# Kernel tuning notes

Measured on AMD Instinct MI355X. Metric: run time of the kernel, lower is better.

## Reference

```python
import jax, jax.numpy as jnp
import numpy as np

DIM = 256
NUM_HEADS = 8
KERNEL_SIZES = [7, 7]
DILATIONS = [1, 2]
NUM_SPLITS = 2
HEAD_DIM = DIM // NUM_HEADS
SCALE = HEAD_DIM ** -0.5


def _window_start(L, K, D):
    """NATTEN get_window_start, vectorized over indices 0..L-1 (static numpy)."""
    idx = np.arange(L)
    NH = K // 2
    if D <= 1:
        return np.maximum(idx - NH, 0) + (idx + NH >= L) * (L - idx - NH - 1)
    ni = idx - NH * D
    imodd = idx % D
    a = (L // D) * D
    b = L - a
    edge = np.where(imodd < b, L - b + imodd - 2 * NH * D, a + imodd - K * D)
    return np.where(ni < 0, imodd, np.where(idx + NH * D >= L, edge, ni))


def _pb_start(L, K, D):
    """NATTEN get_pb_start (relative position bias offset), static numpy."""
    idx = np.arange(L)
    NH = K // 2
    if D <= 1:
        return NH + (idx < NH) * (NH - idx) + (idx + NH >= L) * (L - idx - 1 - NH)
    return np.where(idx - NH * D < 0, K - 1 - idx // D,
                    np.where(idx + NH * D >= L, (L - idx - 1) // D, NH))


def _natten2d(q, k, v, rpb, K, D):
    # q,k,v: [B,h,H,W,d]; rpb: [h, 2K-1, 2K-1]
    B, h, H, W, d = q.shape
    ki = _window_start(H, K, D)[:, None] + D * np.arange(K)   # [H,K]
    kj = _window_start(W, K, D)[:, None] + D * np.arange(K)   # [W,K]
    bi = _pb_start(H, K, D)[:, None] + np.arange(K)           # [H,K]
    bj = _pb_start(W, K, D)[:, None] + np.arange(K)           # [W,K]
    kg = jnp.take(jnp.take(k, ki, axis=2), kj, axis=4)        # [B,h,H,K,W,K,d]
    vg = jnp.take(jnp.take(v, ki, axis=2), kj, axis=4)        # [B,h,H,K,W,K,d]
    attn = jnp.einsum('bhijd,bhiujvd->bhijuv', q, kg)         # [B,h,H,W,K,K]
    bias = jnp.take(jnp.take(rpb, bi, axis=1), bj, axis=3)    # [h,H,K,W,K]
    attn = attn + bias.transpose(0, 1, 3, 2, 4)[None]
    attn = jax.nn.softmax(attn.reshape(B, h, H, W, K * K), axis=-1)
    attn = attn.reshape(B, h, H, W, K, K)
    return jnp.einsum('bhijuv,bhiujvd->bhijd', attn, vg)      # [B,h,H,W,d]


def setup_inputs() -> dict:
    key = jax.random.key(0)
    ks = jax.random.split(key, 6)
    B, C, H, W = 2, DIM, 56, 56
    x = jax.random.normal(ks[0], (B, C, H, W), dtype=jnp.float32)
    w_qkv1 = jax.random.normal(ks[1], (3 * C, C), dtype=jnp.float32) * (C ** -0.5)
    w_qkv2 = jax.random.normal(ks[2], (3 * C, 1, 3, 3), dtype=jnp.float32) * (1.0 / 3.0)
    rpb0 = jax.random.truncated_normal(ks[3], -2.0, 2.0,
                                       (NUM_HEADS // NUM_SPLITS, 13, 13), dtype=jnp.float32) * 0.02
    rpb1 = jax.random.truncated_normal(ks[4], -2.0, 2.0,
                                       (NUM_HEADS // NUM_SPLITS, 13, 13), dtype=jnp.float32) * 0.02
    w_proj = jax.random.normal(ks[5], (C, C), dtype=jnp.float32) * (C ** -0.5)
    return {"x": x, "w_qkv1": w_qkv1, "w_qkv2": w_qkv2,
            "rpb0": rpb0, "rpb1": rpb1, "w_proj": w_proj}


def reference(x, w_qkv1, w_qkv2, rpb0, rpb1, w_proj):
    B, C, H, W = x.shape
    # qkv: 1x1 conv (no bias) then depthwise 3x3 conv (no bias)
    y = jnp.einsum('oc,bchw->bohw', w_qkv1, x)
    y = jax.lax.conv_general_dilated(
        y, w_qkv2, window_strides=(1, 1), padding='SAME',
        dimension_numbers=('NCHW', 'OIHW', 'NCHW'), feature_group_count=3 * C)
    # Faithful to torch: raw reshape of [B,3C,H,W] -> [B,H,W,3,nh,hd]
    qkv = y.reshape(B, H, W, 3, NUM_HEADS, HEAD_DIM).transpose(3, 0, 4, 1, 2, 5)
    q, k, v = qkv[0] * SCALE, qkv[1], qkv[2]   # [B,nh,H,W,hd]
    hs = NUM_HEADS // NUM_SPLITS
    rpbs = [rpb0, rpb1]
    outs = []
    for s in range(NUM_SPLITS):
        sl = slice(s * hs, (s + 1) * hs)
        outs.append(_natten2d(q[:, sl], k[:, sl], v[:, sl],
                              rpbs[s], KERNEL_SIZES[s], DILATIONS[s]))
    o = jnp.concatenate(outs, axis=1)                 # [B,nh,H,W,hd]
    o = o.transpose(0, 1, 4, 2, 3).reshape(B, C, H, W)
    return jnp.einsum('oc,bchw->bohw', w_proj, o)
```

## Files before the change

### kernel.cpp

```cpp
#include <hip/hip_runtime.h>
#include <hip/hip_bf16.h>

#define HGT 56
#define WID 56
#define SPA 3136
#define CCH 256
#define C3  768
#define NH  8
#define HD  32
#define YB  2408448
#define ISTR 43008
#define JSTR 768
#define SCALE_Q 0.17677669529663687f

typedef __attribute__((ext_vector_type(8))) short short8;
typedef __attribute__((ext_vector_type(4))) float f32x4;

static __device__ __forceinline__ unsigned short f2bf_bits(float f) {
    __hip_bfloat16 h = __float2bfloat16(f);
    union { __hip_bfloat16 h; unsigned short u; } cv; cv.h = h; return cv.u;
}
static __device__ __forceinline__ float bf_lo(unsigned u) {
    union { unsigned x; float f; } c; c.x = u << 16; return c.f;
}
static __device__ __forceinline__ float bf_hi(unsigned u) {
    union { unsigned x; float f; } c; c.x = u & 0xffff0000u; return c.f;
}
static __device__ __forceinline__ float bfu(unsigned short u) {
    union { unsigned x; float f; } c; c.x = (unsigned)u << 16; return c.f;
}

__global__ __launch_bounds__(256) void k_cvt(const float* __restrict__ x,
                                             const float* __restrict__ w1,
                                             const float* __restrict__ wp,
                                             __hip_bfloat16* __restrict__ xT,
                                             __hip_bfloat16* __restrict__ w1b,
                                             __hip_bfloat16* __restrict__ wpb) {
    __shared__ __align__(16) __hip_bfloat16 Sl[64][80];
    const int t = threadIdx.x;
    const int z = blockIdx.z;
    if (z == 2) {
        const int gid = (blockIdx.y * 49 + blockIdx.x) * 256 + t;
        for (int i = gid * 4; i < 262144; i += 200704) {
            const float* src;
            __hip_bfloat16* dst;
            if (i < 196608) { src = w1 + i; dst = w1b + i; }
            else            { src = wp + (i - 196608); dst = wpb + (i - 196608); }
            float4 v = *(const float4*)src;
            ushort4 u;
            u.x = f2bf_bits(v.x); u.y = f2bf_bits(v.y);
            u.z = f2bf_bits(v.z); u.w = f2bf_bits(v.w);
            *(ushort4*)dst = u;
        }
        return;
    }
    const int b = z, c0 = blockIdx.y * 64, s0 = blockIdx.x * 64;
    const float* xb = x + (size_t)b * (CCH * SPA);
    const int sq = (t & 15) * 4, cq = (t >> 4) * 4;
    float4 r[4];
#pragma unroll
    for (int rr = 0; rr < 4; ++rr)
        r[rr] = *(const float4*)&xb[(size_t)(c0 + cq + rr) * SPA + s0 + sq];
#pragma unroll
    for (int j = 0; j < 4; ++j) {
        ushort4 u;
        u.x = f2bf_bits(((const float*)&r[0])[j]);
        u.y = f2bf_bits(((const float*)&r[1])[j]);
        u.z = f2bf_bits(((const float*)&r[2])[j]);
        u.w = f2bf_bits(((const float*)&r[3])[j]);
        *(ushort4*)&Sl[sq + j][cq] = u;
    }
    __syncthreads();
    const int srow = t >> 2, cslot = t & 3;
    __hip_bfloat16* dst = &xT[(size_t)b * SPA * CCH + (size_t)(s0 + srow) * CCH + c0];
    short8 v0 = *(const short8*)&Sl[srow][cslot * 8];
    short8 v1 = *(const short8*)&Sl[srow][(cslot + 4) * 8];
    *(short8*)&dst[cslot * 8] = v0;
    *(short8*)&dst[(cslot + 4) * 8] = v1;
}

template<bool OBF>
__global__ __launch_bounds__(256) void k_gemm(const __hip_bfloat16* __restrict__ A,
                                              const __hip_bfloat16* __restrict__ B,
                                              void* __restrict__ Cv, int M) {
    __shared__ __align__(16) short sA[4096];
    __shared__ __align__(16) short sB[4096];
    const int t = threadIdx.x;
    const int lane = t & 63, w = t >> 6;
    const int s0 = blockIdx.x * 64, o0 = blockIdx.y * 64, b = blockIdx.z;
    const __hip_bfloat16* Bb = B + (size_t)b * SPA * CCH;

    const int srow = t >> 3;
    const int scol = (t & 7) ^ (srow & 7);
    const char* gA = (const char*)(A  + (size_t)(o0 + srow) * CCH) + scol * 16;
    const char* gB = (const char*)(Bb + (size_t)(s0 + srow) * CCH) + scol * 16;
    char* lA = (char*)sA + w * 1024;
    char* lB = (char*)sB + w * 1024;

    const int wm = w >> 1, wn = w & 1;
    const int lr = lane & 15, kh = lane >> 4;
    const int ar0 = wm * 32 + lr, ar1 = ar0 + 16;
    const int br0 = wn * 32 + lr, br1 = br0 + 16;

    f32x4 acc[2][2] = {};
    for (int kt = 0; kt < 4; ++kt) {
        __builtin_amdgcn_global_load_lds(
            (const __attribute__((address_space(1))) void*)(gA + kt * 128),
            (__attribute__((address_space(3))) void*)lA, 16, 0, 0);
        __builtin_amdgcn_global_load_lds(
            (const __attribute__((address_space(1))) void*)(gA + 16384 + kt * 128),
            (__attribute__((address_space(3))) void*)(lA + 4096), 16, 0, 0);
        __builtin_amdgcn_global_load_lds(
            (const __attribute__((address_space(1))) void*)(gB + kt * 128),
            (__attribute__((address_space(3))) void*)lB, 16, 0, 0);
        __builtin_amdgcn_global_load_lds(
            (const __attribute__((address_space(1))) void*)(gB + 16384 + kt * 128),
            (__attribute__((address_space(3))) void*)(lB + 4096), 16, 0, 0);
        __syncthreads();
#pragma unroll
        for (int kk = 0; kk < 2; ++kk) {
            const int kg = (kk << 2) | kh;
            short8 a0 = *(const short8*)&sA[(ar0 * 128 + ((kg ^ (ar0 & 7)) << 4)) >> 1];
            short8 a1 = *(const short8*)&sA[(ar1 * 128 + ((kg ^ (ar1 & 7)) << 4)) >> 1];
            short8 b0 = *(const short8*)&sB[(br0 * 128 + ((kg ^ (br0 & 7)) << 4)) >> 1];
            short8 b1 = *(const short8*)&sB[(br1 * 128 + ((kg ^ (br1 & 7)) << 4)) >> 1];
            acc[0][0] = __builtin_amdgcn_mfma_f32_16x16x32_bf16(a0, b0, acc[0][0], 0, 0, 0);
            acc[0][1] = __builtin_amdgcn_mfma_f32_16x16x32_bf16(a0, b1, acc[0][1], 0, 0, 0);
            acc[1][0] = __builtin_amdgcn_mfma_f32_16x16x32_bf16(a1, b0, acc[1][0], 0, 0, 0);
            acc[1][1] = __builtin_amdgcn_mfma_f32_16x16x32_bf16(a1, b1, acc[1][1], 0, 0, 0);
        }
        __syncthreads();
    }
#pragma unroll
    for (int mi = 0; mi < 2; ++mi)
#pragma unroll
        for (int ni = 0; ni < 2; ++ni) {
            const int r0 = o0 + wm * 32 + mi * 16 + kh * 4;
            const int cc = s0 + wn * 32 + ni * 16 + lr;
            if constexpr (OBF) {
                __hip_bfloat16* Cb = (__hip_bfloat16*)Cv + (size_t)b * M * SPA;
#pragma unroll
                for (int q = 0; q < 4; ++q)
                    Cb[(size_t)(r0 + q) * SPA + cc] = __float2bfloat16(acc[mi][ni][q]);
            } else {
                float* Cb = (float*)Cv + (size_t)b * M * SPA;
#pragma unroll
                for (int q = 0; q < 4; ++q)
                    Cb[(size_t)(r0 + q) * SPA + cc] = acc[mi][ni][q];
            }
        }
}

__global__ __launch_bounds__(256) void k_dw(const __hip_bfloat16* __restrict__ y1,
                                            const float* __restrict__ w2,
                                            __hip_bfloat16* __restrict__ y2) {
    int idx = blockIdx.x * 256 + threadIdx.x;
    int tw = idx % 14;
    int rest = idx / 14;
    int h = rest % HGT;
    int bc = rest / HGT;
    int w0 = tw * 4;
    const __hip_bfloat16* in = y1 + (size_t)bc * SPA;
    const float* wt = w2 + (bc % C3) * 9;
    float a0 = 0.f, a1 = 0.f, a2 = 0.f, a3 = 0.f;
#pragma unroll
    for (int dh = -1; dh <= 1; ++dh) {
        int hh = h + dh;
        if (hh < 0 || hh >= HGT) continue;
        const __hip_bfloat16* rp = in + hh * WID + w0;
        ushort4 c4 = *(const ushort4*)rp;
        float c0 = bfu(c4.x), c1 = bfu(c4.y), c2 = bfu(c4.z), c3 = bfu(c4.w);
        float l = (w0 > 0)  ? bfu(*(const unsigned short*)(rp - 1)) : 0.f;
        float r = (w0 < 52) ? bfu(*(const unsigned short*)(rp + 4)) : 0.f;
        float wl = wt[(dh + 1) * 3 + 0];
        float wc = wt[(dh + 1) * 3 + 1];
        float wr = wt[(dh + 1) * 3 + 2];
        a0 += wl * l  + wc * c0 + wr * c1;
        a1 += wl * c0 + wc * c1 + wr * c2;
        a2 += wl * c1 + wc * c2 + wr * c3;
        a3 += wl * c2 + wc * c3 + wr * r;
    }
    ushort4 o;
    o.x = f2bf_bits(a0); o.y = f2bf_bits(a1);
    o.z = f2bf_bits(a2); o.w = f2bf_bits(a3);
    *(ushort4*)(y2 + (size_t)bc * SPA + h * WID + w0) = o;
}

template<int D>
__device__ __forceinline__ void attn_body(short* __restrict__ Kl,
                                          short* __restrict__ Vl,
                                          float* __restrict__ biasl,
                                          int* __restrict__ cpvt,
                                          const __hip_bfloat16* __restrict__ y2,
                                          const float* __restrict__ rpb,
                                          __hip_bfloat16* __restrict__ opre,
                                          int b, int head, int i, int half_, int hsub) {
    const int tid = threadIdx.x;
    const int lane = tid & 63, wid = tid >> 6;
    const int cmin = half_ ? 21 : 0;

    int wsi, pbi;
    if (D == 1) {
        wsi = (i < 3) ? 0 : ((i > 52) ? 49 : i - 3);
        pbi = (i < 3) ? 6 - i : ((i > 52) ? 55 - i : 3);
    } else {
        wsi = (i < 6) ? (i & 1) : ((i >= 50) ? 42 + (i & 1) : i - 6);
        pbi = (i < 6) ? 6 - (i >> 1) : ((i >= 50) ? (55 - i) >> 1 : 3);
    }

    const __hip_bfloat16* ybase = y2 + (size_t)b * YB + head * HD;

    const __hip_bfloat16* kbase = ybase + CCH     + wsi * ISTR + cmin * JSTR;
    const __hip_bfloat16* vbase = ybase + 2 * CCH + wsi * ISTR + cmin * JSTR;
    for (int f = tid; f < 1960; f += 256) {
        const bool isV = f >= 980;
        const int g = isV ? f - 980 : f;
        const int col = g / 28;
        const int rem = g - col * 28;
        const int u = rem >> 2, r = rem & 3;
        const __hip_bfloat16* src = (isV ? vbase : kbase) + u * (D * ISTR) + col * JSTR + r * 8;
        short8 s = *(const short8*)src;
        const int colS = (!isV && D == 2) ? ((col >> 1) + (col & 1) * 18) : col;
        short* dst = isV ? Vl : Kl;
        *(short8*)&dst[(colS * 7 + u) * 40 + r * 8] = s;
    }
    if (tid < 169) biasl[tid] = rpb[hsub * 169 + tid];
    if (tid < 52) {
        int uu = tid / 7, vv = tid - uu * 7;
        cpvt[tid] = (tid < 49) ? (D * vv * 7 + uu) * 20 : 0;
    }
    __syncthreads();

    int u = lane / 7, v = lane - u * 7;
    const bool act = lane < 49;
    if (!act) { u = 0; v = 0; }
    const int bconst = u * 13 + v + pbi * 13;
    const int qt = lane >> 4, dp = lane & 15;
    const unsigned* Vw = (const unsigned*)Vl;

    int cpw[13];
#pragma unroll
    for (int t = 0; t < 13; ++t) cpw[t] = cpvt[qt * 13 + t];

    const int j0 = half_ * 28 + wid * 7;
    const size_t obase = (size_t)b * (SPA * CCH) + (size_t)(i * WID) * CCH + head * HD + dp * 2;

    float qA[32], qB[32];
    float eA, eB;
    int kA, kB;

    auto loadq = [&](float (&dst)[32], int jx) {
        const short8* qp = (const short8*)(ybase + i * ISTR + jx * JSTR);
#pragma unroll
        for (int r = 0; r < 4; ++r) {
            short8 tq = qp[r];
            const unsigned* tu = (const unsigned*)&tq;
#pragma unroll
            for (int e = 0; e < 4; ++e) {
                dst[8 * r + 2 * e]     = bf_lo(tu[e]);
                dst[8 * r + 2 * e + 1] = bf_hi(tu[e]);
            }
        }
    };

    auto phase1 = [&](const float (&q)[32], int j, float& eo, int& ko) {
        int wsj, pbj;
        if (D == 1) {
            wsj = (j < 3) ? 0 : ((j > 52) ? 49 : j - 3);
            pbj = (j < 3) ? 6 - j : ((j > 52) ? 55 - j : 3);
        } else {
            wsj = (j < 6) ? (j & 1) : ((j >= 50) ? 42 + (j & 1) : j - 6);
            pbj = (j < 6) ? 6 - (j >> 1) : ((j >= 50) ? (55 - j) >> 1 : 3);
        }
        const int kcol0 = wsj - cmin;
        ko = kcol0;
        int rrl;
        if (D == 1) rrl = (kcol0 + v) * 7 + u;
        else {
            const int kc = kcol0 + 2 * v;
            rrl = ((kc >> 1) + (kc & 1) * 18) * 7 + u;
        }
        const short* kp = &Kl[rrl * 40];
        float a0 = 0.f, a1 = 0.f;
#pragma unroll
        for (int s = 0; s < 4; ++s) {
            short8 kk = *(const short8*)(kp + s * 8);
            const unsigned* ku = (const unsigned*)&kk;
            float& ac = (s < 2) ? a0 : a1;
#pragma unroll
            for (int e = 0; e < 4; ++e) {
                ac += q[s * 8 + 2 * e]     * bf_lo(ku[e]);
                ac += q[s * 8 + 2 * e + 1] * bf_hi(ku[e]);
            }
        }
        eo = act ? __expf((a0 + a1) * SCALE_Q + biasl[bconst + pbj]) : 0.f;
    };

    auto phase2 = [&](float ev, int kc, int jx) {
        const int vbw = kc * 140 + dp;
        float o0 = 0.f, o1 = 0.f;
#pragma unroll
        for (int t = 0; t < 13; ++t) {
            const float wv = __shfl(ev, qt * 13 + t);
            const unsigned vw = Vw[vbw + cpw[t]];
            o0 += wv * bf_lo(vw);
            o1 += wv * bf_hi(vw);
        }
        float ssum = ev;
#pragma unroll
        for (int off = 32; off; off >>= 1) ssum += __shfl_xor(ssum, off);
        o0 += __shfl_xor(o0, 16); o0 += __shfl_xor(o0, 32);
        o1 += __shfl_xor(o1, 16); o1 += __shfl_xor(o1, 32);
        const float rinv = __frcp_rn(ssum);
        if (lane < 16) {
            union { ushort2 s; unsigned w; } pk;
            pk.s.x = f2bf_bits(o0 * rinv);
            pk.s.y = f2bf_bits(o1 * rinv);
            *(unsigned*)&opre[obase + (size_t)jx * CCH] = pk.w;
        }
    };

    loadq(qA, j0);          phase1(qA, j0,     eA, kA);
    loadq(qB, j0 + 1);      phase1(qB, j0 + 1, eB, kB);  phase2(eA, kA, j0);
    loadq(qA, j0 + 2);      phase1(qA, j0 + 2, eA, kA);  phase2(eB, kB, j0 + 1);
    loadq(qB, j0 + 3);      phase1(qB, j0 + 3, eB, kB);  phase2(eA, kA, j0 + 2);
    loadq(qA, j0 + 4);      phase1(qA, j0 + 4, eA, kA);  phase2(eB, kB, j0 + 3);
    loadq(qB, j0 + 5);      phase1(qB, j0 + 5, eB, kB);  phase2(eA, kA, j0 + 4);
    loadq(qA, j0 + 6);      phase1(qA, j0 + 6, eA, kA);  phase2(eB, kB, j0 + 5);
    phase2(eA, kA, j0 + 6);
}

__global__ __launch_bounds__(256) void k_attn6(const __hip_bfloat16* __restrict__ y2,
                                               const float* __restrict__ rpb0,
                                               const float* __restrict__ rpb1,
                                               __hip_bfloat16* __restrict__ opre) {
    __shared__ __align__(16) short Kl[9800];
    __shared__ __align__(16) short Vl[9800];
    __shared__ float biasl[169];
    __shared__ int   cpvt[52];
    const int half_ = blockIdx.x;
    const int i = blockIdx.y;
    const int bh = blockIdx.z;
    const int b = bh >> 3, head = bh & 7;
    if (head < 4)
        attn_body<1>(Kl, Vl, biasl, cpvt, y2, rpb0, opre, b, head, i, half_, head);
    else
        attn_body<2>(Kl, Vl, biasl, cpvt, y2, rpb1, opre, b, head, i, half_, head - 4);
}

extern "C" void kernel_launch(void* const* d_in, const int* in_sizes, int n_in,
                              void* d_out, int out_size, void* d_ws, size_t ws_size,
                              hipStream_t stream) {
    const float* x    = (const float*)d_in[0];
    const float* w1   = (const float*)d_in[1];
    const float* w2   = (const float*)d_in[2];
    const float* rpb0 = (const float*)d_in[3];
    const float* rpb1 = (const float*)d_in[4];
    const float* wp   = (const float*)d_in[5];
    float* out = (float*)d_out;

    float* p = (float*)d_ws;
    __hip_bfloat16* y1b  = (__hip_bfloat16*)p;
    __hip_bfloat16* y2b  = (__hip_bfloat16*)(p + YB);
    __hip_bfloat16* xT   = (__hip_bfloat16*)(p + 2 * YB);
    __hip_bfloat16* opre = xT;
    __hip_bfloat16* w1b  = (__hip_bfloat16*)(p + 2 * YB + 802816);
    __hip_bfloat16* wpb  = (__hip_bfloat16*)(p + 2 * YB + 802816 + 98304);

    k_cvt<<<dim3(49, 4, 3), 256, 0, stream>>>(x, w1, wp, xT, w1b, wpb);
    k_gemm<true><<<dim3(49, 12, 2), 256, 0, stream>>>(w1b, xT, (void*)y1b, C3);
    k_dw<<<dim3(4704), 256, 0, stream>>>(y1b, w2, y2b);
    k_attn6<<<dim3(2, HGT, 2 * NH), 256, 0, stream>>>(y2b, rpb0, rpb1, opre);
    k_gemm<false><<<dim3(49, 4, 2), 256, 0, stream>>>(wpb, opre, (void*)out, CCH);
}
```

Before: 63.85 us.

## Rewrite neighborhood attention kernel to use MFMA over full key rows

The attention kernel is restructured so each block handles a whole image row. QK^T and PV are computed with bf16 16x16x32 MFMA over all 56 key columns per window row, with out-of-window entries masked to zero. K and Q are staged via direct global-to-LDS loads with XOR swizzles, V is transposed into LDS, and the exponentiated bias is precomputed. This trades scalar FMA and shuffle work for dense matrix ops, at the cost of redundant computation on masked positions, more LDS, fewer blocks and a per-window-row block barrier.

```diff
diff --git a/kernel.cpp b/kernel.cpp
--- a/kernel.cpp
+++ b/kernel.cpp
@@ -28,6 +28,9 @@
 }
 static __device__ __forceinline__ float bfu(unsigned short u) {
     union { unsigned x; float f; } c; c.x = (unsigned)u << 16; return c.f;
+}
+static __device__ __forceinline__ unsigned pk2bf(float a, float b) {
+    return ((unsigned)f2bf_bits(b) << 16) | (unsigned)f2bf_bits(a);
 }
 
 __global__ __launch_bounds__(256) void k_cvt(const float* __restrict__ x,
@@ -187,17 +190,18 @@
 }
 
 template<int D>
-__device__ __forceinline__ void attn_body(short* __restrict__ Kl,
-                                          short* __restrict__ Vl,
-                                          float* __restrict__ biasl,
-                                          int* __restrict__ cpvt,
-                                          const __hip_bfloat16* __restrict__ y2,
-                                          const float* __restrict__ rpb,
-                                          __hip_bfloat16* __restrict__ opre,
-                                          int b, int head, int i, int half_, int hsub) {
+__device__ __forceinline__ void attn7_body(short* __restrict__ sK,
+                                           short* __restrict__ sVT,
+                                           short* __restrict__ sQ,
+                                           short* __restrict__ sP,
+                                           float* __restrict__ sEB,
+                                           const __hip_bfloat16* __restrict__ y2,
+                                           const float* __restrict__ rpb,
+                                           __hip_bfloat16* __restrict__ opre,
+                                           int b, int head, int i, int hsub) {
     const int tid = threadIdx.x;
-    const int lane = tid & 63, wid = tid >> 6;
-    const int cmin = half_ ? 21 : 0;
+    const int lane = tid & 63, w = tid >> 6;
+    const int lr = lane & 15, kh = lane >> 4;
 
     int wsi, pbi;
     if (D == 1) {
@@ -208,144 +212,155 @@
         pbi = (i < 6) ? 6 - (i >> 1) : ((i >= 50) ? (55 - i) >> 1 : 3);
     }
 
-    const __hip_bfloat16* ybase = y2 + (size_t)b * YB + head * HD;
-
-    const __hip_bfloat16* kbase = ybase + CCH     + wsi * ISTR + cmin * JSTR;
-    const __hip_bfloat16* vbase = ybase + 2 * CCH + wsi * ISTR + cmin * JSTR;
-    for (int f = tid; f < 1960; f += 256) {
-        const bool isV = f >= 980;
-        const int g = isV ? f - 980 : f;
-        const int col = g / 28;
-        const int rem = g - col * 28;
-        const int u = rem >> 2, r = rem & 3;
-        const __hip_bfloat16* src = (isV ? vbase : kbase) + u * (D * ISTR) + col * JSTR + r * 8;
-        short8 s = *(const short8*)src;
-        const int colS = (!isV && D == 2) ? ((col >> 1) + (col & 1) * 18) : col;
-        short* dst = isV ? Vl : Kl;
-        *(short8*)&dst[(colS * 7 + u) * 40 + r * 8] = s;
-    }
-    if (tid < 169) biasl[tid] = rpb[hsub * 169 + tid];
-    if (tid < 52) {
-        int uu = tid / 7, vv = tid - uu * 7;
-        cpvt[tid] = (tid < 49) ? (D * vv * 7 + uu) * 20 : 0;
+    const __hip_bfloat16* base  = y2 + (size_t)b * YB + head * HD;
+    const __hip_bfloat16* kbase = base + CCH     + wsi * ISTR;
+    const __hip_bfloat16* vbase = base + 2 * CCH + wsi * ISTR;
+    const __hip_bfloat16* qbase = base + i * ISTR;
+
+    for (int f = tid; f < 1792; f += 256) {
+        int u = f >> 8, rem = f & 255, kj = rem >> 2, slot = rem & 3;
+        int kjc = (kj > 55) ? 55 : kj;
+        const __hip_bfloat16* src = kbase + u * (D * ISTR) + kjc * JSTR + ((slot ^ (kj & 3)) << 3);
+        char* dst = (char*)sK + (size_t)(f - lane) * 16;
+        __builtin_amdgcn_global_load_lds(
+            (const __attribute__((address_space(1))) void*)src,
+            (__attribute__((address_space(3))) void*)dst, 16, 0, 0);
+    }
+    {
+        int jq = tid >> 2, slot = tid & 3;
+        int jqc = (jq > 55) ? 55 : jq;
+        const __hip_bfloat16* src = qbase + jqc * JSTR + ((slot ^ (jq & 3)) << 3);
+        char* dst = (char*)sQ + (size_t)(tid - lane) * 16;
+        __builtin_amdgcn_global_load_lds(
+            (const __attribute__((address_space(1))) void*)src,
+            (__attribute__((address_space(3))) void*)dst, 16, 0, 0);
+    }
+    for (int f = tid; f < 1568; f += 256) {
+        int u = f / 224, rem = f - u * 224;
+        int dq = rem / 28, kjp = rem - dq * 28;
+        const __hip_bfloat16* g0 = vbase + u * (D * ISTR) + (2 * kjp) * JSTR + dq * 4;
+        ushort4 va = *(const ushort4*)g0;
+        ushort4 vb = *(const ushort4*)(g0 + JSTR);
+#pragma unroll
+        for (int e = 0; e < 4; ++e) {
+            int d = dq * 4 + e;
+            unsigned pk = ((unsigned)((&vb.x)[e]) << 16) | (unsigned)((&va.x)[e]);
+            int row = u * 32 + d;
+            int byt = row * 128 + ((((kjp >> 2) ^ (d & 7)) << 4)) + (kjp & 3) * 4;
+            *(unsigned*)((char*)sVT + byt) = pk;
+        }
+    }
+    if (tid < 224) {
+        int u = tid >> 5, d = tid & 31;
+        int row = u * 32 + d;
+        int byt = row * 128 + ((7 ^ (d & 7)) << 4);
+        *(short8*)((char*)sVT + byt) = (short8){0, 0, 0, 0, 0, 0, 0, 0};
+    }
+    if (tid < 91) {
+        int u = tid / 13, r = tid - u * 13;
+        sEB[tid] = __expf(rpb[hsub * 169 + (pbi + u) * 13 + r]);
     }
     __syncthreads();
 
-    int u = lane / 7, v = lane - u * 7;
-    const bool act = lane < 49;
-    if (!act) { u = 0; v = 0; }
-    const int bconst = u * 13 + v + pbi * 13;
-    const int qt = lane >> 4, dp = lane & 15;
-    const unsigned* Vw = (const unsigned*)Vl;
-
-    int cpw[13];
-#pragma unroll
-    for (int t = 0; t < 13; ++t) cpw[t] = cpvt[qt * 13 + t];
-
-    const int j0 = half_ * 28 + wid * 7;
-    const size_t obase = (size_t)b * (SPA * CCH) + (size_t)(i * WID) * CCH + head * HD + dp * 2;
-
-    float qA[32], qB[32];
-    float eA, eB;
-    int kA, kB;
-
-    auto loadq = [&](float (&dst)[32], int jx) {
-        const short8* qp = (const short8*)(ybase + i * ISTR + jx * JSTR);
-#pragma unroll
-        for (int r = 0; r < 4; ++r) {
-            short8 tq = qp[r];
-            const unsigned* tu = (const unsigned*)&tq;
-#pragma unroll
-            for (int e = 0; e < 4; ++e) {
-                dst[8 * r + 2 * e]     = bf_lo(tu[e]);
-                dst[8 * r + 2 * e + 1] = bf_hi(tu[e]);
+    const int j = w * 16 + lr;
+    int wsj;
+    if (D == 1) wsj = (j < 3) ? 0 : ((j > 52) ? 49 : j - 3);
+    else        wsj = (j < 6) ? (j & 1) : ((j >= 50) ? 42 + (j & 1) : j - 6);
+
+    short8 qf = *(const short8*)((char*)sQ + j * 64 + ((kh ^ (j & 3)) << 4));
+
+    float ssum = 0.f;
+    f32x4 oacc0 = {0.f, 0.f, 0.f, 0.f};
+    f32x4 oacc1 = {0.f, 0.f, 0.f, 0.f};
+    short* sPw = sP + w * 2048;
+
+#pragma unroll
+    for (int u = 0; u < 7; ++u) {
+        char* sPb = (char*)(sPw + (u & 1) * 1024);
+        f32x4 s[4];
+#pragma unroll
+        for (int Mt = 0; Mt < 4; ++Mt) {
+            int kjrow = u * 64 + Mt * 16 + lr;
+            short8 kf = *(const short8*)((char*)sK + kjrow * 64 + ((kh ^ (lr & 3)) << 4));
+            s[Mt] = __builtin_amdgcn_mfma_f32_16x16x32_bf16(kf, qf,
+                        (f32x4){0.f, 0.f, 0.f, 0.f}, 0, 0, 0);
+        }
+#pragma unroll
+        for (int Mt = 0; Mt < 4; ++Mt) {
+            const int kjb = Mt * 16 + (kh << 2);
+            float ev[4];
+#pragma unroll
+            for (int q = 0; q < 4; ++q) {
+                int kj = kjb + q;
+                int rel = kj - j;
+                int din = kj - wsj;
+                bool valid = (din >= 0) && (din <= 6 * D);
+                if (D == 2) valid = valid && ((rel & 1) == 0);
+                int r = (D == 1) ? (rel + 6) : ((rel >> 1) + 6);
+                r = r < 0 ? 0 : (r > 12 ? 12 : r);
+                float ex = __expf(s[Mt][q] * SCALE_Q) * sEB[u * 13 + r];
+                ev[q] = valid ? ex : 0.f;
+                ssum += ev[q];
             }
-        }
-    };
-
-    auto phase1 = [&](const float (&q)[32], int j, float& eo, int& ko) {
-        int wsj, pbj;
-        if (D == 1) {
-            wsj = (j < 3) ? 0 : ((j > 52) ? 49 : j - 3);
-            pbj = (j < 3) ? 6 - j : ((j > 52) ? 55 - j : 3);
-        } else {
-            wsj = (j < 6) ? (j & 1) : ((j >= 50) ? 42 + (j & 1) : j - 6);
-            pbj = (j < 6) ? 6 - (j >> 1) : ((j >= 50) ? (55 - j) >> 1 : 3);
-        }
-        const int kcol0 = wsj - cmin;
-        ko = kcol0;
-        int rrl;
-        if (D == 1) rrl = (kcol0 + v) * 7 + u;
-        else {
-            const int kc = kcol0 + 2 * v;
-            rrl = ((kc >> 1) + (kc & 1) * 18) * 7 + u;
-        }
-        const short* kp = &Kl[rrl * 40];
-        float a0 = 0.f, a1 = 0.f;
-#pragma unroll
-        for (int s = 0; s < 4; ++s) {
-            short8 kk = *(const short8*)(kp + s * 8);
-            const unsigned* ku = (const unsigned*)&kk;
-            float& ac = (s < 2) ? a0 : a1;
-#pragma unroll
-            for (int e = 0; e < 4; ++e) {
-                ac += q[s * 8 + 2 * e]     * bf_lo(ku[e]);
-                ac += q[s * 8 + 2 * e + 1] * bf_hi(ku[e]);
+            uint2 pk2;
+            pk2.x = pk2bf(ev[0], ev[1]);
+            pk2.y = pk2bf(ev[2], ev[3]);
+            int g = Mt * 2 + (kh >> 1);
+            int byt = lr * 128 + (((g ^ (lr & 7)) << 4)) + (kh & 1) * 8;
+            *(uint2*)(sPb + byt) = pk2;
+        }
+        __syncthreads();
+#pragma unroll
+        for (int Kt = 0; Kt < 2; ++Kt) {
+            short8 pf = *(const short8*)(sPb + lr * 128 + ((((Kt * 4 + kh) ^ (lr & 7)) << 4)));
+            {
+                int row = u * 32 + lr;
+                short8 vf = *(const short8*)((char*)sVT + row * 128 +
+                              ((((Kt * 4 + kh) ^ (lr & 7)) << 4)));
+                oacc0 = __builtin_amdgcn_mfma_f32_16x16x32_bf16(vf, pf, oacc0, 0, 0, 0);
             }
-        }
-        eo = act ? __expf((a0 + a1) * SCALE_Q + biasl[bconst + pbj]) : 0.f;
-    };
-
-    auto phase2 = [&](float ev, int kc, int jx) {
-        const int vbw = kc * 140 + dp;
-        float o0 = 0.f, o1 = 0.f;
-#pragma unroll
-        for (int t = 0; t < 13; ++t) {
-            const float wv = __shfl(ev, qt * 13 + t);
-            const unsigned vw = Vw[vbw + cpw[t]];
-            o0 += wv * bf_lo(vw);
-            o1 += wv * bf_hi(vw);
-        }
-        float ssum = ev;
-#pragma unroll
-        for (int off = 32; off; off >>= 1) ssum += __shfl_xor(ssum, off);
-        o0 += __shfl_xor(o0, 16); o0 += __shfl_xor(o0, 32);
-        o1 += __shfl_xor(o1, 16); o1 += __shfl_xor(o1, 32);
+            {
+                int row = u * 32 + 16 + lr;
+                short8 vf = *(const short8*)((char*)sVT + row * 128 +
+                              ((((Kt * 4 + kh) ^ (lr & 7)) << 4)));
+                oacc1 = __builtin_amdgcn_mfma_f32_16x16x32_bf16(vf, pf, oacc1, 0, 0, 0);
+            }
+        }
+    }
+
+    ssum += __shfl_xor(ssum, 16);
+    ssum += __shfl_xor(ssum, 32);
+
+    if (j < 56) {
         const float rinv = __frcp_rn(ssum);
-        if (lane < 16) {
-            union { ushort2 s; unsigned w; } pk;
-            pk.s.x = f2bf_bits(o0 * rinv);
-            pk.s.y = f2bf_bits(o1 * rinv);
-            *(unsigned*)&opre[obase + (size_t)jx * CCH] = pk.w;
-        }
-    };
-
-    loadq(qA, j0);          phase1(qA, j0,     eA, kA);
-    loadq(qB, j0 + 1);      phase1(qB, j0 + 1, eB, kB);  phase2(eA, kA, j0);
-    loadq(qA, j0 + 2);      phase1(qA, j0 + 2, eA, kA);  phase2(eB, kB, j0 + 1);
-    loadq(qB, j0 + 3);      phase1(qB, j0 + 3, eB, kB);  phase2(eA, kA, j0 + 2);
-    loadq(qA, j0 + 4);      phase1(qA, j0 + 4, eA, kA);  phase2(eB, kB, j0 + 3);
-    loadq(qB, j0 + 5);      phase1(qB, j0 + 5, eB, kB);  phase2(eA, kA, j0 + 4);
-    loadq(qA, j0 + 6);      phase1(qA, j0 + 6, eA, kA);  phase2(eB, kB, j0 + 5);
-    phase2(eA, kA, j0 + 6);
-}
-
-__global__ __launch_bounds__(256) void k_attn6(const __hip_bfloat16* __restrict__ y2,
+        const size_t ob = (size_t)b * (SPA * CCH) + (size_t)(i * WID + j) * CCH
+                          + head * HD + (kh << 2);
+        uint2 p0, p1;
+        p0.x = pk2bf(oacc0[0] * rinv, oacc0[1] * rinv);
+        p0.y = pk2bf(oacc0[2] * rinv, oacc0[3] * rinv);
+        p1.x = pk2bf(oacc1[0] * rinv, oacc1[1] * rinv);
+        p1.y = pk2bf(oacc1[2] * rinv, oacc1[3] * rinv);
+        *(uint2*)&opre[ob]      = p0;
+        *(uint2*)&opre[ob + 16] = p1;
+    }
+}
+
+__global__ __launch_bounds__(256) void k_attn7(const __hip_bfloat16* __restrict__ y2,
                                                const float* __restrict__ rpb0,
                                                const float* __restrict__ rpb1,
                                                __hip_bfloat16* __restrict__ opre) {
-    __shared__ __align__(16) short Kl[9800];
-    __shared__ __align__(16) short Vl[9800];
-    __shared__ float biasl[169];
-    __shared__ int   cpvt[52];
-    const int half_ = blockIdx.x;
-    const int i = blockIdx.y;
-    const int bh = blockIdx.z;
+    __shared__ __align__(16) short sK[14336];
+    __shared__ __align__(16) short sVT[14336];
+    __shared__ __align__(16) short sQ[2048];
+    __shared__ __align__(16) short sP[8192];
+    __shared__ float sEB[91];
+    const int i = blockIdx.x;
+    const int bh = blockIdx.y;
     const int b = bh >> 3, head = bh & 7;
     if (head < 4)
-        attn_body<1>(Kl, Vl, biasl, cpvt, y2, rpb0, opre, b, head, i, half_, head);
+        attn7_body<1>(sK, sVT, sQ, sP, sEB, y2, rpb0, opre, b, head, i, head);
     else
-        attn_body<2>(Kl, Vl, biasl, cpvt, y2, rpb1, opre, b, head, i, half_, head - 4);
+        attn7_body<2>(sK, sVT, sQ, sP, sEB, y2, rpb1, opre, b, head, i, head - 4);
 }
 
 extern "C" void kernel_launch(void* const* d_in, const int* in_sizes, int n_in,
@@ -370,6 +385,6 @@
     k_cvt<<<dim3(49, 4, 3), 256, 0, stream>>>(x, w1, wp, xT, w1b, wpb);
     k_gemm<true><<<dim3(49, 12, 2), 256, 0, stream>>>(w1b, xT, (void*)y1b, C3);
     k_dw<<<dim3(4704), 256, 0, stream>>>(y1b, w2, y2b);
-    k_attn6<<<dim3(2, HGT, 2 * NH), 256, 0, stream>>>(y2b, rpb0, rpb1, opre);
+    k_attn7<<<dim3(HGT, 2 * NH), 256, 0, stream>>>(y2b, rpb0, rpb1, opre);
     k_gemm<false><<<dim3(49, 4, 2), 256, 0, stream>>>(wpb, opre, (void*)out, CCH);
 }
```

Result: faster. 58.53 us (-8.3%).
